# Optimization experiments

Measured on AMD Instinct MI355X. Metric: run time of the kernel, lower is better.

## Reference

```python
import jax, jax.numpy as jnp
import numpy as np

N_NODES = 20000
N_EDGES = 40000
N_GRAPHS = 500
D_IN = 32     # initial_dim_gcn
D_E = 16      # edge_dim_feature
H1 = 100      # hidden_dim_nn_1
H2 = 20       # hidden_dim_nn_2
F1 = 50       # hidden_dim_fcn_1


def setup_inputs() -> dict:
    key = jax.random.key(0)
    ks = jax.random.split(key, 16)
    s = lambda k, shp, fan: (jax.random.normal(k, shp, jnp.float32) / np.sqrt(fan)).astype(jnp.float32)
    return {
        "x": jax.random.normal(ks[0], (N_NODES, D_IN), jnp.float32),
        "edge_attr": jax.random.normal(ks[1], (N_EDGES, D_E), jnp.float32),
        "edge_index": jax.random.randint(ks[2], (2, N_EDGES), 0, N_NODES, jnp.int64),
        "batch": jnp.sort(jax.random.randint(ks[3], (N_NODES,), 0, N_GRAPHS, jnp.int64)),
        # NNConv layer 1: edge MLP Linear(D_E -> D_IN*H1), root weight, bias
        "nn1_W": s(ks[4], (D_E, D_IN * H1), D_E),
        "nn1_b": jnp.zeros((D_IN * H1,), jnp.float32),
        "root1": s(ks[5], (D_IN, H1), D_IN),
        "bias1": jnp.zeros((H1,), jnp.float32),
        # NNConv layer 2: edge MLP Linear(D_E -> H1*H2), root weight, bias
        "nn2_W": s(ks[6], (D_E, H1 * H2), D_E),
        "nn2_b": jnp.zeros((H1 * H2,), jnp.float32),
        "root2": s(ks[7], (H1, H2), H1),
        "bias2": jnp.zeros((H2,), jnp.float32),
        # FCN head
        "lin1_W": s(ks[8], (H2, F1), H2),
        "lin1_b": jnp.zeros((F1,), jnp.float32),
        "lin2_W": s(ks[9], (F1, 1), F1),
        "lin2_b": jnp.zeros((1,), jnp.float32),
    }


def _nnconv(x, src, dst, edge_attr, nnW, nnb, root, bias, d_in, d_out):
    # per-edge weight matrices: [E, d_in, d_out]
    theta = (edge_attr @ nnW + nnb).reshape(-1, d_in, d_out)
    # gather source features, per-edge matmul, scatter-add to targets
    msg = jnp.einsum('ei,eio->eo', x[src], theta)            # [E, d_out]
    agg = jax.ops.segment_sum(msg, dst, num_segments=x.shape[0])
    return agg + x @ root + bias


def reference(x, edge_attr, edge_index, batch,
              nn1_W, nn1_b, root1, bias1,
              nn2_W, nn2_b, root2, bias2,
              lin1_W, lin1_b, lin2_W, lin2_b):
    src, dst = edge_index[0], edge_index[1]  # PyG: message from j=src, aggregate at i=dst
    h = jax.nn.relu(_nnconv(x, src, dst, edge_attr, nn1_W, nn1_b, root1, bias1, D_IN, H1))
    h = jax.nn.relu(_nnconv(h, src, dst, edge_attr, nn2_W, nn2_b, root2, bias2, H1, H2))
    g = jax.ops.segment_sum(h, batch, num_segments=N_GRAPHS)  # sum-pool readout [G, H2]
    g = jax.nn.relu(g @ lin1_W + lin1_b)
    out = g @ lin2_W + lin2_b
    return out.reshape(-1)
```

## Files before the change

kernel.cpp:

```cpp
#include <hip/hip_runtime.h>
#include <hip/hip_bf16.h>
#include <hip/hip_fp16.h>

#define N_NODES 20000
#define N_EDGES 40000
#define N_GRAPHS 500
#define D_IN 32
#define D_E 16
#define H1 100
#define H2 20
#define F1 50

#define EB 128
#define YNB 12
#define ET3 12

using h2f = __attribute__((ext_vector_type(2))) _Float16;
using h8f = __attribute__((ext_vector_type(8))) _Float16;
using f4  = __attribute__((ext_vector_type(4))) float;

__global__ __launch_bounds__(256) void prep_kernel(
    const float* __restrict__ nn1W, const float* __restrict__ nn1b,
    const float* __restrict__ nn2W, const float* __restrict__ nn2b,
    unsigned short* __restrict__ Wfrag, float* __restrict__ Bext)
{
  const int tid = blockIdx.x * 256 + threadIdx.x;
  if (tid < 544 * 112) {
    const int c  = tid / 3584;
    const int r  = tid % 3584;
    const int to = r / 512;
    const int l  = (r % 512) >> 3;
    const int j  = r & 7;
    const int i  = (l >> 4) * 8 + j;
    const int o  = to * 16 + (l & 15);
    float v = 0.f;
    if (o < H1) v = (c < 16) ? nn1W[c * (D_IN * H1) + i * H1 + o] : nn1b[i * H1 + o];
    _Float16 hv = (_Float16)v;
    Wfrag[tid] = __builtin_bit_cast(unsigned short, hv);
  } else {
    const int idx = tid - 544 * 112;
    if (idx < H1 * 340) {
      const int i = idx / 340, j = idx % 340;
      const int k = j / H2, o = j % H2;
      Bext[idx] = (k < 16) ? nn2W[k * (H1 * H2) + i * H2 + o] : nn2b[i * H2 + o];
    }
  }
}

__global__ __launch_bounds__(256) void edge1_kernel(
    const float* __restrict__ x, const float* __restrict__ ea,
    const int* __restrict__ eidx, const unsigned short* __restrict__ Wfrag,
    float* __restrict__ agg1)
{
  __shared__ uint4 Plds[8 * 64];
  __shared__ int   sdst[EB];

  const int t    = threadIdx.x;
  const int lane = t & 63;
  const int w    = t >> 6;
  const int e0   = blockIdx.x * EB;

  const int e_loc = t >> 1;
  const int ih    = t & 1;
  const int ec    = min(e0 + e_loc, N_EDGES - 1);
  const int src   = eidx[ec];

  h2f xh[8];
  {
    const float4* xp = (const float4*)&x[(size_t)src * D_IN + ih * 16];
    float4 v0 = xp[0], v1 = xp[1], v2 = xp[2], v3 = xp[3];
    float xf[16] = {v0.x,v0.y,v0.z,v0.w, v1.x,v1.y,v1.z,v1.w,
                    v2.x,v2.y,v2.z,v2.w, v3.x,v3.y,v3.z,v3.w};
    #pragma unroll
    for (int j = 0; j < 8; ++j) {
      h2f p; p[0] = (_Float16)xf[2*j]; p[1] = (_Float16)xf[2*j+1]; xh[j] = p;
    }
  }
  _Float16 eh[17];
  {
    const float4* ep = (const float4*)&ea[(size_t)ec * D_E];
    float4 v0 = ep[0], v1 = ep[1], v2 = ep[2], v3 = ep[3];
    float ef[16] = {v0.x,v0.y,v0.z,v0.w, v1.x,v1.y,v1.z,v1.w,
                    v2.x,v2.y,v2.z,v2.w, v3.x,v3.y,v3.z,v3.w};
    #pragma unroll
    for (int k = 0; k < 16; ++k) eh[k] = (_Float16)ef[k];
    eh[16] = (_Float16)1.0f;
  }
  if (t < EB) sdst[t] = eidx[N_EDGES + min(e0 + t, N_EDGES - 1)];
  __syncthreads();

  f4 acc[2][7];
  #pragma unroll
  for (int te = 0; te < 2; ++te)
    #pragma unroll
    for (int to = 0; to < 7; ++to)
      acc[te][to] = f4{0.f, 0.f, 0.f, 0.f};

  const uint4* __restrict__ Bf = (const uint4*)Wfrag;
  const int etw   = 2 * w;
  const int pbase = (e_loc >> 4) * 64 + (e_loc & 15) + 16 * (2 * ih);

  #pragma unroll
  for (int c = 0; c < 17; ++c) {
    const uint4* bc = Bf + c * 448 + lane;
    uint4 b0 = bc[0*64], b1 = bc[1*64], b2 = bc[2*64], b3 = bc[3*64];
    uint4 b4 = bc[4*64], b5 = bc[5*64], b6 = bc[6*64];

    h2f es; es[0] = eh[c]; es[1] = eh[c];
    unsigned int pk[8];
    #pragma unroll
    for (int j = 0; j < 8; ++j) {
      h2f pr = xh[j] * es;
      pk[j] = __builtin_bit_cast(unsigned int, pr);
    }
    Plds[pbase]      = make_uint4(pk[0], pk[1], pk[2], pk[3]);
    Plds[pbase + 16] = make_uint4(pk[4], pk[5], pk[6], pk[7]);

    uint4 a0 = Plds[ etw      * 64 + lane];
    uint4 a1 = Plds[(etw + 1) * 64 + lane];
    h8f A0 = __builtin_bit_cast(h8f, a0);
    h8f A1 = __builtin_bit_cast(h8f, a1);

    uint4 bb[7] = {b0, b1, b2, b3, b4, b5, b6};
    #pragma unroll
    for (int to = 0; to < 7; ++to) {
      h8f B = __builtin_bit_cast(h8f, bb[to]);
      acc[0][to] = __builtin_amdgcn_mfma_f32_16x16x32_f16(A0, B, acc[0][to], 0, 0, 0);
      acc[1][to] = __builtin_amdgcn_mfma_f32_16x16x32_f16(A1, B, acc[1][to], 0, 0, 0);
    }
  }

  const int col = lane & 15, rowg = lane >> 4;
  #pragma unroll
  for (int te = 0; te < 2; ++te) {
    #pragma unroll
    for (int r = 0; r < 4; ++r) {
      const int el = (etw + te) * 16 + rowg * 4 + r;
      if (e0 + el < N_EDGES) {
        const int d = sdst[el];
        float* ap = agg1 + (size_t)d * H1;
        #pragma unroll
        for (int to = 0; to < 7; ++to) {
          const int o = to * 16 + col;
          if (o < H1) atomicAdd(&ap[o], acc[te][to][r]);
        }
      }
    }
  }
}

__global__ __launch_bounds__(128) void node1_kernel(
    const float* __restrict__ x, const float* __restrict__ agg1,
    const float* __restrict__ root1, const float* __restrict__ bias1,
    float* __restrict__ h1)
{
  __shared__ float sx[D_IN];
  const int n = blockIdx.x;
  const int o = threadIdx.x;
  if (o < D_IN) sx[o] = x[n * D_IN + o];
  __syncthreads();
  if (o < H1) {
    float v = agg1[n * H1 + o] + bias1[o];
    #pragma unroll
    for (int i = 0; i < D_IN; ++i) v = fmaf(sx[i], root1[i * H1 + o], v);
    h1[n * H1 + o] = fmaxf(v, 0.f);
  }
}

__global__ __launch_bounds__(256) void y2_kernel(
    const float* __restrict__ h1, const float* __restrict__ Bext,
    float* __restrict__ Y2)
{
  __shared__ __align__(16) float hT[H1][YNB];
  const int t  = threadIdx.x;
  const int n0 = blockIdx.x * YNB;

  for (int idx = t; idx < YNB * H1; idx += 256) {
    const int nn = idx / H1, i = idx - nn * H1;
    const int n = n0 + nn;
    hT[i][nn] = (n < N_NODES) ? h1[(size_t)n * H1 + i] : 0.f;
  }
  __syncthreads();

  const int jg = t % 85;
  const int ng = t / 85;
  if (ng < 3) {
    const int j0 = jg * 4;
    const float* __restrict__ bp = Bext + j0;
    float acc[4][4];
    #pragma unroll
    for (int r = 0; r < 4; ++r)
      #pragma unroll
      for (int c = 0; c < 4; ++c) acc[r][c] = 0.f;

    #pragma unroll 2
    for (int i = 0; i < H1; ++i) {
      const float4 bv = *(const float4*)&bp[i * 340];
      const float4 hv = *(const float4*)&hT[i][ng * 4];
      acc[0][0] = fmaf(hv.x, bv.x, acc[0][0]);
      acc[0][1] = fmaf(hv.x, bv.y, acc[0][1]);
      acc[0][2] = fmaf(hv.x, bv.z, acc[0][2]);
      acc[0][3] = fmaf(hv.x, bv.w, acc[0][3]);
      acc[1][0] = fmaf(hv.y, bv.x, acc[1][0]);
      acc[1][1] = fmaf(hv.y, bv.y, acc[1][1]);
      acc[1][2] = fmaf(hv.y, bv.z, acc[1][2]);
      acc[1][3] = fmaf(hv.y, bv.w, acc[1][3]);
      acc[2][0] = fmaf(hv.z, bv.x, acc[2][0]);
      acc[2][1] = fmaf(hv.z, bv.y, acc[2][1]);
      acc[2][2] = fmaf(hv.z, bv.z, acc[2][2]);
      acc[2][3] = fmaf(hv.z, bv.w, acc[2][3]);
      acc[3][0] = fmaf(hv.w, bv.x, acc[3][0]);
      acc[3][1] = fmaf(hv.w, bv.y, acc[3][1]);
      acc[3][2] = fmaf(hv.w, bv.z, acc[3][2]);
      acc[3][3] = fmaf(hv.w, bv.w, acc[3][3]);
    }
    const int nb = n0 + ng * 4;
    #pragma unroll
    for (int r = 0; r < 4; ++r) {
      const int n = nb + r;
      if (n < N_NODES)
        *(float4*)&Y2[(size_t)n * 340 + j0] =
            make_float4(acc[r][0], acc[r][1], acc[r][2], acc[r][3]);
    }
  }
}

__global__ __launch_bounds__(256) void edge2_kernel(
    const float* __restrict__ ea, const int* __restrict__ eidx,
    const float* __restrict__ Y2, float* __restrict__ agg2)
{
  __shared__ __align__(16) float sy[ET3][344];
  __shared__ float se[ET3][16];
  __shared__ int sd[ET3];
  const int t  = threadIdx.x;
  const int e0 = blockIdx.x * ET3;

  if (t < ET3) {
    const int e = e0 + t;
    sd[t] = (e < N_EDGES) ? eidx[N_EDGES + e] : -1;
  }
  for (int idx = t; idx < ET3 * 4; idx += 256) {
    const int el = idx >> 2, q = idx & 3;
    const int e = e0 + el;
    if (e < N_EDGES)
      *(float4*)&se[el][q * 4] = *(const float4*)&ea[(size_t)e * D_E + q * 4];
  }
  for (int idx = t; idx < ET3 * 85; idx += 256) {
    const int el = idx / 85, q = idx - el * 85;
    const int e = e0 + el;
    if (e < N_EDGES) {
      const int s = eidx[e];
      *(float4*)&sy[el][q * 4] = *(const float4*)&Y2[(size_t)s * 340 + q * 4];
    }
  }
  __syncthreads();

  const int el = t / H2, o = t % H2;
  const int e = e0 + el;
  if (el < ET3 && e < N_EDGES) {
    float m = sy[el][320 + o];
    #pragma unroll
    for (int k = 0; k < D_E; ++k)
      m = fmaf(se[el][k], sy[el][k * 20 + o], m);
    atomicAdd(&agg2[(size_t)sd[el] * H2 + o], m);
  }
}

__global__ __launch_bounds__(256) void node2_pool_kernel(
    const float* __restrict__ h1, const float* __restrict__ agg2,
    const float* __restrict__ root2, const float* __restrict__ bias2,
    const int* __restrict__ batch, float* __restrict__ g)
{
  __shared__ float sroot[H1 * H2];
  __shared__ float sv[ET3][H2];
  __shared__ int   sg[ET3];
  const int t  = threadIdx.x;
  const int n0 = blockIdx.x * ET3;

  for (int idx = t; idx < (H1 * H2) / 4; idx += 256)
    *(float4*)&sroot[idx * 4] = *(const float4*)&root2[idx * 4];
  if (t < ET3) {
    const int n = n0 + t;
    sg[t] = (n < N_NODES) ? batch[n] : -1;
  }
  __syncthreads();

  const int nl = t / H2, o = t % H2;
  const int n = n0 + nl;
  if (nl < ET3) {
    float v = 0.f;
    if (n < N_NODES) {
      v = agg2[(size_t)n * H2 + o] + bias2[o];
      const float* hr = &h1[(size_t)n * H1];
      #pragma unroll 5
      for (int i = 0; i < H1; i += 4) {
        const float4 hv = *(const float4*)&hr[i];
        v = fmaf(hv.x, sroot[(i    ) * H2 + o], v);
        v = fmaf(hv.y, sroot[(i + 1) * H2 + o], v);
        v = fmaf(hv.z, sroot[(i + 2) * H2 + o], v);
        v = fmaf(hv.w, sroot[(i + 3) * H2 + o], v);
      }
      v = fmaxf(v, 0.f);
    }
    sv[nl][o] = v;
  }
  __syncthreads();

  if (t < H2) {
    float run = 0.f;
    int cur = sg[0];
    #pragma unroll
    for (int r = 0; r < ET3; ++r) {
      const int gid = sg[r];
      if (gid != cur) {
        if (cur >= 0) atomicAdd(&g[cur * H2 + t], run);
        run = 0.f; cur = gid;
      }
      run += sv[r][t];
    }
    if (cur >= 0) atomicAdd(&g[cur * H2 + t], run);
  }
}

__global__ __launch_bounds__(64) void final_kernel(
    const float* __restrict__ g, const float* __restrict__ lin1W,
    const float* __restrict__ lin1b, const float* __restrict__ lin2W,
    const float* __restrict__ lin2b, float* __restrict__ out)
{
  const int gr = blockIdx.x;
  const int tt = threadIdx.x;
  float v = 0.f;
  if (tt < F1) {
    float s = lin1b[tt];
    #pragma unroll
    for (int o = 0; o < H2; ++o) s = fmaf(g[gr * H2 + o], lin1W[o * F1 + tt], s);
    v = fmaxf(s, 0.f) * lin2W[tt];
  }
  #pragma unroll
  for (int off = 32; off > 0; off >>= 1) v += __shfl_down(v, off, 64);
  if (tt == 0) out[gr] = v + lin2b[0];
}

extern "C" void kernel_launch(void* const* d_in, const int* in_sizes, int n_in,
                              void* d_out, int out_size, void* d_ws, size_t ws_size,
                              hipStream_t stream) {
  const float* x     = (const float*)d_in[0];
  const float* ea    = (const float*)d_in[1];
  const int*   eidx  = (const int*)d_in[2];
  const int*   batch = (const int*)d_in[3];
  const float* nn1W  = (const float*)d_in[4];
  const float* nn1b  = (const float*)d_in[5];
  const float* root1 = (const float*)d_in[6];
  const float* bias1 = (const float*)d_in[7];
  const float* nn2W  = (const float*)d_in[8];
  const float* nn2b  = (const float*)d_in[9];
  const float* root2 = (const float*)d_in[10];
  const float* bias2 = (const float*)d_in[11];
  const float* lin1W = (const float*)d_in[12];
  const float* lin1b = (const float*)d_in[13];
  const float* lin2W = (const float*)d_in[14];
  const float* lin2b = (const float*)d_in[15];
  float* out = (float*)d_out;

  float* ws   = (float*)d_ws;
  float* agg1 = ws;
  float* agg2 = agg1 + N_NODES * H1;
  float* g    = agg2 + N_NODES * H2;
  float* h1   = g    + N_GRAPHS * H2;
  float* spare= h1   + N_NODES * H1;
  float* Y2   = spare+ N_NODES * H2;
  float* Bext = spare;
  unsigned short* Wfrag = (unsigned short*)(Y2 + (size_t)N_NODES * 340 - 30464);

  hipMemsetAsync(agg1, 0,
      (size_t)(N_NODES * H1 + N_NODES * H2 + N_GRAPHS * H2) * sizeof(float), stream);

  prep_kernel<<<(544 * 112 + H1 * 340 + 255) / 256, 256, 0, stream>>>(
      nn1W, nn1b, nn2W, nn2b, Wfrag, Bext);
  edge1_kernel<<<(N_EDGES + EB - 1) / EB, 256, 0, stream>>>(x, ea, eidx, Wfrag, agg1);
  node1_kernel<<<N_NODES, 128, 0, stream>>>(x, agg1, root1, bias1, h1);
  y2_kernel<<<(N_NODES + YNB - 1) / YNB, 256, 0, stream>>>(h1, Bext, Y2);
  edge2_kernel<<<(N_EDGES + ET3 - 1) / ET3, 256, 0, stream>>>(ea, eidx, Y2, agg2);
  node2_pool_kernel<<<(N_NODES + ET3 - 1) / ET3, 256, 0, stream>>>(
      h1, agg2, root2, bias2, batch, g);
  final_kernel<<<N_GRAPHS, 64, 0, stream>>>(g, lin1W, lin1b, lin2W, lin2b, out);
}
```

Before: 201.8 us.

## Fuse zeroing into prep, LDS-stage edge1 weights, merge node1 into y2

Measured after the change: 182.7 us. 1.1x faster.

```diff
diff --git a/kernel.cpp b/kernel.cpp
--- a/kernel.cpp
+++ b/kernel.cpp
@@ -11,7 +11,7 @@
 #define H2 20
 #define F1 50
 
-#define EB 128
+#define EB1 64
 #define YNB 12
 #define ET3 12
 
@@ -22,7 +22,8 @@
 __global__ __launch_bounds__(256) void prep_kernel(
     const float* __restrict__ nn1W, const float* __restrict__ nn1b,
     const float* __restrict__ nn2W, const float* __restrict__ nn2b,
-    unsigned short* __restrict__ Wfrag, float* __restrict__ Bext)
+    unsigned short* __restrict__ Wfrag, float* __restrict__ Bext,
+    float* __restrict__ zbase)
 {
   const int tid = blockIdx.x * 256 + threadIdx.x;
   if (tid < 544 * 112) {
@@ -37,48 +38,48 @@
     if (o < H1) v = (c < 16) ? nn1W[c * (D_IN * H1) + i * H1 + o] : nn1b[i * H1 + o];
     _Float16 hv = (_Float16)v;
     Wfrag[tid] = __builtin_bit_cast(unsigned short, hv);
-  } else {
+  } else if (tid < 544 * 112 + H1 * 340) {
     const int idx = tid - 544 * 112;
-    if (idx < H1 * 340) {
-      const int i = idx / 340, j = idx % 340;
-      const int k = j / H2, o = j % H2;
-      Bext[idx] = (k < 16) ? nn2W[k * (H1 * H2) + i * H2 + o] : nn2b[i * H2 + o];
-    }
-  }
-}
-
-__global__ __launch_bounds__(256) void edge1_kernel(
+    const int i = idx / 340, j = idx % 340;
+    const int k = j / H2, o = j % H2;
+    Bext[idx] = (k < 16) ? nn2W[k * (H1 * H2) + i * H2 + o] : nn2b[i * H2 + o];
+  }
+  float4* zp = (float4*)zbase;
+  for (int i = tid; i < 602500; i += 512 * 256)
+    zp[i] = make_float4(0.f, 0.f, 0.f, 0.f);
+}
+
+__global__ __launch_bounds__(256, 2) void edge1_kernel(
     const float* __restrict__ x, const float* __restrict__ ea,
     const int* __restrict__ eidx, const unsigned short* __restrict__ Wfrag,
     float* __restrict__ agg1)
 {
-  __shared__ uint4 Plds[8 * 64];
-  __shared__ int   sdst[EB];
+  __shared__ uint4 Plds[4 * 64];
+  __shared__ uint4 Blds[2][7 * 64];
+  __shared__ int   sdst[EB1];
 
   const int t    = threadIdx.x;
   const int lane = t & 63;
   const int w    = t >> 6;
-  const int e0   = blockIdx.x * EB;
-
-  const int e_loc = t >> 1;
-  const int ih    = t & 1;
-  const int ec    = min(e0 + e_loc, N_EDGES - 1);
-  const int src   = eidx[ec];
-
-  h2f xh[8];
+  const int e0   = blockIdx.x * EB1;
+
+  const int e_loc = t >> 2;
+  const int jg    = t & 3;
+  const int src   = eidx[e0 + e_loc];
+
+  h2f xh[4];
   {
-    const float4* xp = (const float4*)&x[(size_t)src * D_IN + ih * 16];
-    float4 v0 = xp[0], v1 = xp[1], v2 = xp[2], v3 = xp[3];
-    float xf[16] = {v0.x,v0.y,v0.z,v0.w, v1.x,v1.y,v1.z,v1.w,
-                    v2.x,v2.y,v2.z,v2.w, v3.x,v3.y,v3.z,v3.w};
-    #pragma unroll
-    for (int j = 0; j < 8; ++j) {
+    const float4* xp = (const float4*)&x[(size_t)src * D_IN + jg * 8];
+    float4 v0 = xp[0], v1 = xp[1];
+    float xf[8] = {v0.x, v0.y, v0.z, v0.w, v1.x, v1.y, v1.z, v1.w};
+    #pragma unroll
+    for (int j = 0; j < 4; ++j) {
       h2f p; p[0] = (_Float16)xf[2*j]; p[1] = (_Float16)xf[2*j+1]; xh[j] = p;
     }
   }
   _Float16 eh[17];
   {
-    const float4* ep = (const float4*)&ea[(size_t)ec * D_E];
+    const float4* ep = (const float4*)&ea[(size_t)(e0 + e_loc) * D_E];
     float4 v0 = ep[0], v1 = ep[1], v2 = ep[2], v3 = ep[3];
     float ef[16] = {v0.x,v0.y,v0.z,v0.w, v1.x,v1.y,v1.z,v1.w,
                     v2.x,v2.y,v2.z,v2.w, v3.x,v3.y,v3.z,v3.w};
@@ -86,99 +87,110 @@
     for (int k = 0; k < 16; ++k) eh[k] = (_Float16)ef[k];
     eh[16] = (_Float16)1.0f;
   }
-  if (t < EB) sdst[t] = eidx[N_EDGES + min(e0 + t, N_EDGES - 1)];
-  __syncthreads();
-
-  f4 acc[2][7];
+  if (t < EB1) sdst[t] = eidx[N_EDGES + e0 + t];
+
+  const uint4* __restrict__ Bf = (const uint4*)Wfrag;
+
+  {
+    uint4 s0 = Bf[t];
+    uint4 s1;
+    if (t < 192) s1 = Bf[256 + t];
+    Blds[0][t] = s0;
+    if (t < 192) Blds[0][256 + t] = s1;
+  }
+  __syncthreads();
+
+  f4 acc[7];
   #pragma unroll
-  for (int te = 0; te < 2; ++te)
-    #pragma unroll
-    for (int to = 0; to < 7; ++to)
-      acc[te][to] = f4{0.f, 0.f, 0.f, 0.f};
-
-  const uint4* __restrict__ Bf = (const uint4*)Wfrag;
-  const int etw   = 2 * w;
-  const int pbase = (e_loc >> 4) * 64 + (e_loc & 15) + 16 * (2 * ih);
+  for (int to = 0; to < 7; ++to) acc[to] = f4{0.f, 0.f, 0.f, 0.f};
+
+  const int pslot = w * 64 + (e_loc & 15) + 16 * jg;
 
   #pragma unroll
   for (int c = 0; c < 17; ++c) {
-    const uint4* bc = Bf + c * 448 + lane;
-    uint4 b0 = bc[0*64], b1 = bc[1*64], b2 = bc[2*64], b3 = bc[3*64];
-    uint4 b4 = bc[4*64], b5 = bc[5*64], b6 = bc[6*64];
+    uint4 s0, s1;
+    if (c < 16) {
+      const uint4* bn = Bf + (c + 1) * 448;
+      s0 = bn[t];
+      if (t < 192) s1 = bn[256 + t];
+    }
 
     h2f es; es[0] = eh[c]; es[1] = eh[c];
-    unsigned int pk[8];
-    #pragma unroll
-    for (int j = 0; j < 8; ++j) {
+    unsigned int pk[4];
+    #pragma unroll
+    for (int j = 0; j < 4; ++j) {
       h2f pr = xh[j] * es;
       pk[j] = __builtin_bit_cast(unsigned int, pr);
     }
-    Plds[pbase]      = make_uint4(pk[0], pk[1], pk[2], pk[3]);
-    Plds[pbase + 16] = make_uint4(pk[4], pk[5], pk[6], pk[7]);
-
-    uint4 a0 = Plds[ etw      * 64 + lane];
-    uint4 a1 = Plds[(etw + 1) * 64 + lane];
-    h8f A0 = __builtin_bit_cast(h8f, a0);
-    h8f A1 = __builtin_bit_cast(h8f, a1);
-
-    uint4 bb[7] = {b0, b1, b2, b3, b4, b5, b6};
+    Plds[pslot] = make_uint4(pk[0], pk[1], pk[2], pk[3]);
+
+    uint4 a = Plds[w * 64 + lane];
+    h8f A = __builtin_bit_cast(h8f, a);
+
+    const uint4* bb = &Blds[c & 1][0];
     #pragma unroll
     for (int to = 0; to < 7; ++to) {
-      h8f B = __builtin_bit_cast(h8f, bb[to]);
-      acc[0][to] = __builtin_amdgcn_mfma_f32_16x16x32_f16(A0, B, acc[0][to], 0, 0, 0);
-      acc[1][to] = __builtin_amdgcn_mfma_f32_16x16x32_f16(A1, B, acc[1][to], 0, 0, 0);
-    }
+      h8f B = __builtin_bit_cast(h8f, bb[to * 64 + lane]);
+      acc[to] = __builtin_amdgcn_mfma_f32_16x16x32_f16(A, B, acc[to], 0, 0, 0);
+    }
+
+    if (c < 16) {
+      Blds[(c + 1) & 1][t] = s0;
+      if (t < 192) Blds[(c + 1) & 1][256 + t] = s1;
+    }
+    __syncthreads();
   }
 
   const int col = lane & 15, rowg = lane >> 4;
   #pragma unroll
-  for (int te = 0; te < 2; ++te) {
-    #pragma unroll
-    for (int r = 0; r < 4; ++r) {
-      const int el = (etw + te) * 16 + rowg * 4 + r;
-      if (e0 + el < N_EDGES) {
-        const int d = sdst[el];
-        float* ap = agg1 + (size_t)d * H1;
-        #pragma unroll
-        for (int to = 0; to < 7; ++to) {
-          const int o = to * 16 + col;
-          if (o < H1) atomicAdd(&ap[o], acc[te][to][r]);
-        }
-      }
-    }
-  }
-}
-
-__global__ __launch_bounds__(128) void node1_kernel(
+  for (int r = 0; r < 4; ++r) {
+    const int el = w * 16 + rowg * 4 + r;
+    const int d = sdst[el];
+    float* ap = agg1 + (size_t)d * H1;
+    #pragma unroll
+    for (int to = 0; to < 7; ++to) {
+      const int o = to * 16 + col;
+      if (o < H1) atomicAdd(&ap[o], acc[to][r]);
+    }
+  }
+}
+
+__global__ __launch_bounds__(256) void y2h1_kernel(
     const float* __restrict__ x, const float* __restrict__ agg1,
     const float* __restrict__ root1, const float* __restrict__ bias1,
-    float* __restrict__ h1)
-{
-  __shared__ float sx[D_IN];
-  const int n = blockIdx.x;
-  const int o = threadIdx.x;
-  if (o < D_IN) sx[o] = x[n * D_IN + o];
-  __syncthreads();
-  if (o < H1) {
-    float v = agg1[n * H1 + o] + bias1[o];
-    #pragma unroll
-    for (int i = 0; i < D_IN; ++i) v = fmaf(sx[i], root1[i * H1 + o], v);
-    h1[n * H1 + o] = fmaxf(v, 0.f);
-  }
-}
-
-__global__ __launch_bounds__(256) void y2_kernel(
-    const float* __restrict__ h1, const float* __restrict__ Bext,
+    const float* __restrict__ Bext, float* __restrict__ h1,
     float* __restrict__ Y2)
 {
+  __shared__ float sroot1[D_IN * H1];
+  __shared__ float sxl[YNB * D_IN];
   __shared__ __align__(16) float hT[H1][YNB];
   const int t  = threadIdx.x;
   const int n0 = blockIdx.x * YNB;
 
+  for (int idx = t; idx < 800; idx += 256)
+    *(float4*)&sroot1[idx * 4] = *(const float4*)&root1[idx * 4];
+  if (t < 96) {
+    const int fo = t * 4;
+    const int nn = fo >> 5;
+    float4 v = make_float4(0.f, 0.f, 0.f, 0.f);
+    if (n0 + nn < N_NODES) v = *(const float4*)&x[(size_t)n0 * D_IN + fo];
+    *(float4*)&sxl[fo] = v;
+  }
+  __syncthreads();
+
   for (int idx = t; idx < YNB * H1; idx += 256) {
     const int nn = idx / H1, i = idx - nn * H1;
     const int n = n0 + nn;
-    hT[i][nn] = (n < N_NODES) ? h1[(size_t)n * H1 + i] : 0.f;
+    float v = 0.f;
+    if (n < N_NODES) {
+      v = agg1[(size_t)n0 * H1 + idx] + bias1[i];
+      #pragma unroll 8
+      for (int d = 0; d < D_IN; ++d)
+        v = fmaf(sxl[nn * D_IN + d], sroot1[d * H1 + i], v);
+      v = fmaxf(v, 0.f);
+      h1[(size_t)n0 * H1 + idx] = v;
+    }
+    hT[i][nn] = v;
   }
   __syncthreads();
 
@@ -191,7 +203,7 @@
     #pragma unroll
     for (int r = 0; r < 4; ++r)
       #pragma unroll
-      for (int c = 0; c < 4; ++c) acc[r][c] = 0.f;
+      for (int cc = 0; cc < 4; ++cc) acc[r][cc] = 0.f;
 
     #pragma unroll 2
     for (int i = 0; i < H1; ++i) {
@@ -372,14 +384,10 @@
   float* Bext = spare;
   unsigned short* Wfrag = (unsigned short*)(Y2 + (size_t)N_NODES * 340 - 30464);
 
-  hipMemsetAsync(agg1, 0,
-      (size_t)(N_NODES * H1 + N_NODES * H2 + N_GRAPHS * H2) * sizeof(float), stream);
-
-  prep_kernel<<<(544 * 112 + H1 * 340 + 255) / 256, 256, 0, stream>>>(
-      nn1W, nn1b, nn2W, nn2b, Wfrag, Bext);
-  edge1_kernel<<<(N_EDGES + EB - 1) / EB, 256, 0, stream>>>(x, ea, eidx, Wfrag, agg1);
-  node1_kernel<<<N_NODES, 128, 0, stream>>>(x, agg1, root1, bias1, h1);
-  y2_kernel<<<(N_NODES + YNB - 1) / YNB, 256, 0, stream>>>(h1, Bext, Y2);
+  prep_kernel<<<512, 256, 0, stream>>>(nn1W, nn1b, nn2W, nn2b, Wfrag, Bext, agg1);
+  edge1_kernel<<<N_EDGES / EB1, 256, 0, stream>>>(x, ea, eidx, Wfrag, agg1);
+  y2h1_kernel<<<(N_NODES + YNB - 1) / YNB, 256, 0, stream>>>(
+      x, agg1, root1, bias1, Bext, h1, Y2);
   edge2_kernel<<<(N_EDGES + ET3 - 1) / ET3, 256, 0, stream>>>(ea, eidx, Y2, agg2);
   node2_pool_kernel<<<(N_NODES + ET3 - 1) / ET3, 256, 0, stream>>>(
       h1, agg2, root2, bias2, batch, g);
```
